# Optimization experiments

Hardware: AMD Instinct MI355X
Metric: run time of the kernel (lower is better)

Reference implementation:

```python
import jax, jax.numpy as jnp
import numpy as np

N_NODES = 100000


def _graph_conv(x, W, b, src, dst, inv_sqrt_out, inv_sqrt_in):
    # DGL GraphConv, norm='both':  D_in^{-1/2} A D_out^{-1/2} X W + b
    h = x * inv_sqrt_out[:, None]
    if W.shape[0] > W.shape[1]:
        # in_feats > out_feats: transform first (cheaper aggregation)
        h = h @ W
        m = jax.ops.segment_sum(h[src], dst, num_segments=N_NODES)
    else:
        m = jax.ops.segment_sum(h[src], dst, num_segments=N_NODES)
        m = m @ W
    return m * inv_sqrt_in[:, None] + b


def _degree_norms(src, dst):
    ones = jnp.ones(src.shape[0], dtype=jnp.float32)
    out_deg = jax.ops.segment_sum(ones, src, num_segments=N_NODES)
    in_deg = jax.ops.segment_sum(ones, dst, num_segments=N_NODES)
    # DGL clamps degree to min 1 (allow_zero_in_degree)
    return jnp.clip(out_deg, 1.0) ** -0.5, jnp.clip(in_deg, 1.0) ** -0.5


def setup_inputs() -> dict:
    key = jax.random.key(0)
    ks = jax.random.split(key, 8)
    E = 800000
    in_feats, h1, h2, nc = 128, 256, 128, 40
    return {
        "features": jax.random.normal(ks[0], (N_NODES, in_feats), dtype=jnp.float32),
        "src": jax.random.randint(ks[1], (E,), 0, N_NODES),
        "dst": jax.random.randint(ks[2], (E,), 0, N_NODES),
        "W1": jax.random.normal(ks[3], (in_feats, h1), dtype=jnp.float32) * (2.0 / (in_feats + h1)) ** 0.5,
        "b1": jnp.zeros((h1,), dtype=jnp.float32),
        "W2": jax.random.normal(ks[4], (h1, h2), dtype=jnp.float32) * (2.0 / (h1 + h2)) ** 0.5,
        "b2": jnp.zeros((h2,), dtype=jnp.float32),
        "W3": jax.random.normal(ks[5], (h2, nc), dtype=jnp.float32) * (2.0 / (h2 + nc)) ** 0.5,
        "b3": jnp.zeros((nc,), dtype=jnp.float32),
    }


def reference(features, src, dst, W1, b1, W2, b2, W3, b3):
    inv_out, inv_in = _degree_norms(src, dst)
    h = _graph_conv(features, W1, b1, src, dst, inv_out, inv_in)
    h = jax.nn.relu(h)
    h = _graph_conv(h, W2, b2, src, dst, inv_out, inv_in)
    h = jax.nn.relu(h)
    return _graph_conv(h, W3, b3, src, dst, inv_out, inv_in)
```

## Files before the change

kernel.cpp:

```cpp
#include <hip/hip_runtime.h>

#define N_NODES 100000
#define SCAN_NB 128
#define SCAN_TPB 256
#define GCOUNT 8
#define BINS 12500
#define NSLICE 32

typedef _Float16 half_t;
typedef __attribute__((ext_vector_type(8))) _Float16 v8h;
typedef __attribute__((ext_vector_type(4))) _Float16 v4h;
typedef __attribute__((ext_vector_type(4))) float v4f;


__global__ __launch_bounds__(512) void hist_all(
    const int* __restrict__ src, const int* __restrict__ dst,
    int* __restrict__ loc, unsigned short* __restrict__ partialI,
    unsigned short* __restrict__ partialO, int E,
    const float* __restrict__ W1, const float* __restrict__ W2,
    const float* __restrict__ W3, half_t* __restrict__ Wt1,
    half_t* __restrict__ Wt2, half_t* __restrict__ Wt3) {
    __shared__ int hist[BINS];
    const int bid = blockIdx.x;
    const int tid = threadIdx.x;
    if (bid < 2 * GCOUNT * NSLICE) {
        const bool isDst = bid < GCOUNT * NSLICE;
        const int b2 = isDst ? bid : bid - GCOUNT * NSLICE;
        const int g = b2 >> 5, s = b2 & (NSLICE - 1);
        const int gbase = g * BINS;
        for (int b = tid; b < BINS; b += 512) hist[b] = 0;
        __syncthreads();
        const int chunk = (E + NSLICE - 1) / NSLICE;
        const int e0 = s * chunk;
        const int e1 = min(e0 + chunk, E);
        if (isDst) {
            for (int e = e0 + tid; e < e1; e += 512) {
                int d = dst[e];
                unsigned lb = (unsigned)(d - gbase);
                if (lb < (unsigned)BINS) loc[e] = atomicAdd(&hist[lb], 1);
            }
        } else {
            for (int e = e0 + tid; e < e1; e += 512) {
                int d = src[e];
                unsigned lb = (unsigned)(d - gbase);
                if (lb < (unsigned)BINS) atomicAdd(&hist[lb], 1);
            }
        }
        __syncthreads();
        unsigned short* p = (isDst ? partialI : partialO) + (size_t)b2 * BINS;
        for (int b = tid; b < BINS; b += 512) p[b] = (unsigned short)hist[b];
    } else {
        int u = (bid - 2 * GCOUNT * NSLICE) * 512 + tid;
        if (u < 32768) {
            int n = u >> 7, k = u & 127;
            Wt1[u] = (half_t)W1[(size_t)k * 256 + n];
        } else if (u < 65536) {
            int w = u - 32768;
            int n = w >> 8, k = w & 255;
            Wt2[w] = (half_t)W2[(size_t)k * 128 + n];
        } else if (u < 70656) {
            int w = u - 65536;
            int n = w >> 7, k = w & 127;
            Wt3[w] = (half_t)W3[(size_t)k * 40 + n];
        }
    }
}


__global__ __launch_bounds__(SCAN_TPB) void scan_reduce(
    const unsigned short* __restrict__ partialI, int* __restrict__ blockSum, int n) {
    __shared__ int s[SCAN_TPB];
    int chunk = (n + SCAN_NB - 1) / SCAN_NB;
    int beg = blockIdx.x * chunk;
    int end = min(beg + chunk, n);
    int sum = 0;
    for (int i = beg + threadIdx.x; i < end; i += SCAN_TPB) {
        int g = i / BINS, lb = i - g * BINS;
        const unsigned short* p = partialI + (size_t)g * NSLICE * BINS + lb;
#pragma unroll
        for (int sl = 0; sl < NSLICE; ++sl) sum += p[(size_t)sl * BINS];
    }
    s[threadIdx.x] = sum;
    __syncthreads();
    for (int off = SCAN_TPB / 2; off > 0; off >>= 1) {
        if (threadIdx.x < off) s[threadIdx.x] += s[threadIdx.x + off];
        __syncthreads();
    }
    if (threadIdx.x == 0) blockSum[blockIdx.x] = s[0];
}

__global__ __launch_bounds__(SCAN_NB) void scan_offsets(int* __restrict__ blockSum,
                                                        int* __restrict__ rowptr_total) {
    __shared__ int s[SCAN_NB];
    int tid = threadIdx.x;
    int v = blockSum[tid];
    s[tid] = v;
    __syncthreads();
    for (int off = 1; off < SCAN_NB; off <<= 1) {
        int t = (tid >= off) ? s[tid - off] : 0;
        __syncthreads();
        s[tid] += t;
        __syncthreads();
    }
    blockSum[tid] = s[tid] - v;
    if (tid == SCAN_NB - 1) rowptr_total[0] = s[tid];
}

__global__ __launch_bounds__(SCAN_TPB) void scan_final(
    unsigned short* __restrict__ partialI, const unsigned short* __restrict__ partialO,
    const int* __restrict__ blockSum, int* __restrict__ rowptr,
    float* __restrict__ invIn, float* __restrict__ invOut, int n) {
    __shared__ int s[SCAN_TPB];
    int chunk = (n + SCAN_NB - 1) / SCAN_NB;
    int beg = blockIdx.x * chunk;
    int end = min(beg + chunk, n);
    int carry = blockSum[blockIdx.x];
    for (int base = beg; base < end; base += SCAN_TPB) {
        int i = base + threadIdx.x;
        int v = 0, o = 0;
        if (i < end) {
            int g = i / BINS, lb = i - g * BINS;
            unsigned short* p = partialI + (size_t)g * NSLICE * BINS + lb;
            int run = 0;
#pragma unroll
            for (int sl = 0; sl < NSLICE; ++sl) {
                int c = p[(size_t)sl * BINS];
                p[(size_t)sl * BINS] = (unsigned short)run;
                run += c;
            }
            v = run;
            const unsigned short* q = partialO + (size_t)g * NSLICE * BINS + lb;
#pragma unroll
            for (int sl = 0; sl < NSLICE; ++sl) o += q[(size_t)sl * BINS];
        }
        s[threadIdx.x] = v;
        __syncthreads();
        for (int off = 1; off < SCAN_TPB; off <<= 1) {
            int t = (threadIdx.x >= off) ? s[threadIdx.x - off] : 0;
            __syncthreads();
            s[threadIdx.x] += t;
            __syncthreads();
        }
        int excl = s[threadIdx.x] - v;
        if (i < end) {
            rowptr[i] = carry + excl;
            invOut[i] = rsqrtf((float)max(o, 1));
            invIn[i] = rsqrtf((float)max(v, 1));
        }
        int roundSum = s[SCAN_TPB - 1];
        __syncthreads();
        carry += roundSum;
    }
}


__global__ void prep2(const int* __restrict__ src, const int* __restrict__ dst,
                      const int* __restrict__ loc,
                      const unsigned short* __restrict__ partialI,
                      const int* __restrict__ rowptr,
                      int* __restrict__ eidx, int E,
                      const float* __restrict__ x, const float* __restrict__ invOut,
                      half_t* __restrict__ xh) {
    int t = blockIdx.x * blockDim.x + threadIdx.x;
    if (t < E) {
        int d = dst[t];
        int chunk = (E + NSLICE - 1) / NSLICE;
        int s = t / chunk;
        int g = d / BINS, lb = d - g * BINS;
        int pre = partialI[(size_t)(g * NSLICE + s) * BINS + lb];
        eidx[rowptr[d] + pre + loc[t]] = src[t];
    } else {
        int u = t - E;
        if (u < N_NODES * 32) {
            int n = u >> 5;
            float4 v = ((const float4*)x)[u];
            float s = invOut[n];
            v4h h;
            h[0] = (half_t)(v.x * s);
            h[1] = (half_t)(v.y * s);
            h[2] = (half_t)(v.z * s);
            h[3] = (half_t)(v.w * s);
            *(v4h*)(xh + (size_t)u * 4) = h;
        }
    }
}


template <int F>
__device__ __forceinline__ void gather_row(const half_t* __restrict__ x,
                                           const int* __restrict__ eidx,
                                           int beg, int end, int c, float* acc) {
    const half_t* __restrict__ xc = x + (size_t)c * 8;
    int n = end - beg;
    if (n <= 0) return;
    int nbat = (n + 3) >> 2;
    int i0 = eidx[beg];
    int i1 = eidx[beg + min(1, n - 1)];
    int i2 = eidx[beg + min(2, n - 1)];
    int i3 = eidx[beg + min(3, n - 1)];
    for (int b = 0; b < nbat; ++b) {
        int j = b * 4;
        v8h v0 = *(const v8h*)(xc + (size_t)i0 * F);
        v8h v1 = *(const v8h*)(xc + (size_t)i1 * F);
        v8h v2 = *(const v8h*)(xc + (size_t)i2 * F);
        v8h v3 = *(const v8h*)(xc + (size_t)i3 * F);
        if (b + 1 < nbat) {
            int jn = j + 4;
            i0 = eidx[beg + jn];
            i1 = eidx[beg + min(jn + 1, n - 1)];
            i2 = eidx[beg + min(jn + 2, n - 1)];
            i3 = eidx[beg + min(jn + 3, n - 1)];
        }
        v8h z = (v8h)(half_t)0;
        v1 = (j + 1 < n) ? v1 : z;
        v2 = (j + 2 < n) ? v2 : z;
        v3 = (j + 3 < n) ? v3 : z;
#pragma unroll
        for (int q = 0; q < 8; ++q)
            acc[q] += ((float)v0[q] + (float)v1[q]) + ((float)v2[q] + (float)v3[q]);
    }
}


__global__ __launch_bounds__(256, 8) void gather1(
    const half_t* __restrict__ xh, const int* __restrict__ rowptr,
    const int* __restrict__ eidx, half_t* __restrict__ A1) {
    int t = blockIdx.x * 256 + threadIdx.x;
    int n = t >> 4, c = t & 15;
    if (n >= N_NODES) return;
    float acc[8] = {};
    gather_row<128>(xh, eidx, rowptr[n], rowptr[n + 1], c, acc);
    v8h o;
#pragma unroll
    for (int q = 0; q < 8; ++q) o[q] = (half_t)acc[q];
    *(v8h*)(A1 + (size_t)n * 128 + c * 8) = o;
}

__global__ __launch_bounds__(256, 8) void gather2(
    const half_t* __restrict__ t2, const int* __restrict__ rowptr,
    const int* __restrict__ eidx, const float* __restrict__ invIn,
    const float* __restrict__ invOut, const float* __restrict__ b2,
    half_t* __restrict__ A2) {
    int t = blockIdx.x * 256 + threadIdx.x;
    int n = t >> 4, c = t & 15;
    if (n >= N_NODES) return;
    float acc[8] = {};
    gather_row<128>(t2, eidx, rowptr[n], rowptr[n + 1], c, acc);
    float ii = invIn[n], io = invOut[n];
    float4 blo = ((const float4*)b2)[c * 2];
    float4 bhi = ((const float4*)b2)[c * 2 + 1];
    float bb[8] = {blo.x, blo.y, blo.z, blo.w, bhi.x, bhi.y, bhi.z, bhi.w};
    v8h o;
#pragma unroll
    for (int q = 0; q < 8; ++q)
        o[q] = (half_t)fmaxf((acc[q] * ii + bb[q]) * io, 0.f);
    *(v8h*)(A2 + (size_t)n * 128 + c * 8) = o;
}


__global__ __launch_bounds__(512) void mlp12(
    const half_t* __restrict__ A1, const half_t* __restrict__ Wt1,
    const half_t* __restrict__ Wt2,
    const float* __restrict__ invIn, const float* __restrict__ invOut,
    const float* __restrict__ b1, half_t* __restrict__ t2) {
    constexpr int K1 = 128, K2 = 256, N2 = 128;
    constexpr int LDA = K1 + 8;
    constexpr int LDH = K2 + 8;
    __shared__ half_t As[64][LDA];
    __shared__ half_t h1S[64][LDH];
    __shared__ float iiS[64], ioS[64];
    const int tid = threadIdx.x;
    const int wave = tid >> 6, lane = tid & 63;
    const int quad = lane >> 4, l16 = lane & 15;
    const int m0 = blockIdx.x * 64;
    const int n0 = wave * 32;

    v8h b[2][4];
    float bv[2];
#pragma unroll
    for (int j = 0; j < 2; ++j) {
        int gn = n0 + j * 16 + l16;
        bv[j] = b1[gn];
#pragma unroll
        for (int kc = 0; kc < 4; ++kc)
            b[j][kc] = *(const v8h*)(Wt1 + (size_t)gn * K1 + kc * 32 + quad * 8);
    }
    if (tid < 64) {
        int gm = m0 + tid;
        bool ok = gm < N_NODES;
        iiS[tid] = ok ? invIn[gm] : 0.f;
        ioS[tid] = ok ? invOut[gm] : 0.f;
    }

#pragma unroll
    for (int p = 0; p < 2; ++p) {
        int task = tid + p * 512;
        int r = task >> 4, c = task & 15;
        int gm = m0 + r;
        v8h v = (gm < N_NODES) ? *(const v8h*)(A1 + (size_t)gm * K1 + c * 8)
                               : (v8h)(half_t)0;
        *(v8h*)&As[r][c * 8] = v;
    }
    __syncthreads();

    for (int mt = 0; mt < 4; ++mt) {
        v8h a[4];
#pragma unroll
        for (int kc = 0; kc < 4; ++kc)
            a[kc] = *(const v8h*)&As[mt * 16 + l16][kc * 32 + quad * 8];
        v4f acc[2] = {};
#pragma unroll
        for (int kc = 0; kc < 4; ++kc)
#pragma unroll
            for (int j = 0; j < 2; ++j)
                acc[j] = __builtin_amdgcn_mfma_f32_16x16x32_f16(a[kc], b[j][kc], acc[j], 0, 0, 0);
#pragma unroll
        for (int j = 0; j < 2; ++j) {
            int cn = n0 + j * 16 + l16;
#pragma unroll
            for (int r = 0; r < 4; ++r) {
                int lr = mt * 16 + quad * 4 + r;
                float z = (acc[j][r] * iiS[lr] + bv[j]) * ioS[lr];
                h1S[lr][cn] = (half_t)fmaxf(z, 0.f);
            }
        }
    }

    v8h b2[8];
    const int n02 = wave * 16;
    {
        int gn = n02 + l16;
#pragma unroll
        for (int kc = 0; kc < 8; ++kc)
            b2[kc] = *(const v8h*)(Wt2 + (size_t)gn * K2 + kc * 32 + quad * 8);
    }
    __syncthreads();

    for (int mt = 0; mt < 4; ++mt) {
        v8h a2[8];
#pragma unroll
        for (int kc = 0; kc < 8; ++kc)
            a2[kc] = *(const v8h*)&h1S[mt * 16 + l16][kc * 32 + quad * 8];
        v4f acc2 = {};
#pragma unroll
        for (int kc = 0; kc < 8; ++kc)
            acc2 = __builtin_amdgcn_mfma_f32_16x16x32_f16(a2[kc], b2[kc], acc2, 0, 0, 0);
        int gn = n02 + l16;
#pragma unroll
        for (int r = 0; r < 4; ++r) {
            int gm = m0 + mt * 16 + quad * 4 + r;
            if (gm < N_NODES) t2[(size_t)gm * N2 + gn] = (half_t)acc2[r];
        }
    }
}


__global__ __launch_bounds__(256) void mlp3(
    const half_t* __restrict__ A2, const half_t* __restrict__ Wt3,
    half_t* __restrict__ t3) {
    constexpr int K = 128, N = 40, LDA = K + 8;
    __shared__ half_t As[64][LDA];
    const int tid = threadIdx.x;
    const int wave = tid >> 6, lane = tid & 63;
    const int quad = lane >> 4, l16 = lane & 15;
    const int m0 = blockIdx.x * 64;

    v8h b[3][4];
#pragma unroll
    for (int j = 0; j < 3; ++j) {
        int gn = j * 16 + l16;
#pragma unroll
        for (int kc = 0; kc < 4; ++kc)
            b[j][kc] = (gn < N) ? *(const v8h*)(Wt3 + (size_t)gn * K + kc * 32 + quad * 8)
                                : (v8h)(half_t)0;
    }

#pragma unroll
    for (int p = 0; p < 4; ++p) {
        int task = tid + p * 256;
        int r = task >> 4, c = task & 15;
        int gm = m0 + r;
        v8h v = (gm < N_NODES) ? *(const v8h*)(A2 + (size_t)gm * K + c * 8)
                               : (v8h)(half_t)0;
        *(v8h*)&As[r][c * 8] = v;
    }
    __syncthreads();

    {
        int mt = wave;
        v8h a[4];
#pragma unroll
        for (int kc = 0; kc < 4; ++kc)
            a[kc] = *(const v8h*)&As[mt * 16 + l16][kc * 32 + quad * 8];
        v4f acc[3] = {};
#pragma unroll
        for (int kc = 0; kc < 4; ++kc)
#pragma unroll
            for (int j = 0; j < 3; ++j)
                acc[j] = __builtin_amdgcn_mfma_f32_16x16x32_f16(a[kc], b[j][kc], acc[j], 0, 0, 0);
#pragma unroll
        for (int j = 0; j < 3; ++j) {
            int gn = j * 16 + l16;
            if (gn >= N) continue;
#pragma unroll
            for (int r = 0; r < 4; ++r) {
                int gm = m0 + mt * 16 + quad * 4 + r;
                if (gm < N_NODES) t3[(size_t)gm * N + gn] = (half_t)acc[j][r];
            }
        }
    }
}


__global__ __launch_bounds__(256, 8) void gather_final(
    const half_t* __restrict__ x,
    const int* __restrict__ rowptr, const int* __restrict__ eidx,
    float* __restrict__ out, const float* __restrict__ invIn,
    const float* __restrict__ bias) {
    constexpr int F = 40, V = 5;
    int t = blockIdx.x * blockDim.x + threadIdx.x;
    int n = t / V;
    int v = t - n * V;
    if (n >= N_NODES) return;
    float acc[8] = {};
    gather_row<F>(x, eidx, rowptr[n], rowptr[n + 1], v, acc);
    float ii = invIn[n];
    float* o = out + (size_t)n * F + v * 8;
#pragma unroll
    for (int q = 0; q < 8; ++q) o[q] = acc[q] * ii + bias[v * 8 + q];
}


extern "C" void kernel_launch(void* const* d_in, const int* in_sizes, int n_in,
                              void* d_out, int out_size, void* d_ws, size_t ws_size,
                              hipStream_t stream) {
    const float* x  = (const float*)d_in[0];
    const int* src  = (const int*)d_in[1];
    const int* dst  = (const int*)d_in[2];
    const float* W1 = (const float*)d_in[3];
    const float* b1 = (const float*)d_in[4];
    const float* W2 = (const float*)d_in[5];
    const float* b2 = (const float*)d_in[6];
    const float* W3 = (const float*)d_in[7];
    const float* b3 = (const float*)d_in[8];
    float* out = (float*)d_out;
    const int E = in_sizes[1];

    char* ws = (char*)d_ws;
    float* inv_out = (float*)ws;
    float* inv_in  = (float*)(ws + 400000);
    int* rowptr    = (int*)(ws + 800000);
    int* eidx      = (int*)(ws + 1600256);
    int* blockSum  = (int*)(ws + 4800256);
    half_t* Wt1    = (half_t*)(ws + 4800768);
    half_t* Wt2    = (half_t*)(ws + 4866304);
    half_t* Wt3    = (half_t*)(ws + 4931840);
    half_t* bufA   = (half_t*)(ws + 5000192);
    half_t* bufB   = (half_t*)(ws + 30600192);
    int* loc = (int*)bufB;
    unsigned short* partialI = (unsigned short*)((char*)bufB + 3200000);
    unsigned short* partialO = partialI + (size_t)GCOUNT * NSLICE * BINS;

    const int NBH = 2 * GCOUNT * NSLICE + (70656 + 511) / 512;
    hist_all<<<NBH, 512, 0, stream>>>(src, dst, loc, partialI, partialO, E,
                                      W1, W2, W3, Wt1, Wt2, Wt3);
    scan_reduce<<<SCAN_NB, SCAN_TPB, 0, stream>>>(partialI, blockSum, N_NODES);
    scan_offsets<<<1, SCAN_NB, 0, stream>>>(blockSum, rowptr + N_NODES);
    scan_final<<<SCAN_NB, SCAN_TPB, 0, stream>>>(partialI, partialO, blockSum, rowptr,
                                                 inv_in, inv_out, N_NODES);
    prep2<<<(E + N_NODES * 32 + 255) / 256, 256, 0, stream>>>(src, dst, loc, partialI,
                                                              rowptr, eidx, E,
                                                              x, inv_out, bufA);

    const int NBG = (N_NODES * 16 + 255) / 256;
    const int NB  = (N_NODES + 63) / 64;

    gather1<<<NBG, 256, 0, stream>>>(bufA, rowptr, eidx, bufB);
    mlp12<<<NB, 512, 0, stream>>>(bufB, Wt1, Wt2, inv_in, inv_out, b1, bufA);
    gather2<<<NBG, 256, 0, stream>>>(bufA, rowptr, eidx, inv_in, inv_out, b2, bufB);
    mlp3<<<NB, 256, 0, stream>>>(bufB, Wt3, bufA);
    gather_final<<<(N_NODES * 5 + 255) / 256, 256, 0, stream>>>(
        bufA, rowptr, eidx, out, inv_in, b3);
}
```

Baseline: 294.4 us.

## Fuse layer-2 gather with layer-3 weight transform into one kernel

Merges gather2 and mlp3 into a single kernel. Each 512-thread block gathers 32 rows into shared memory, then six waves apply the 128x40 MFMA transform. This removes the write and read of the 100000x128 half-precision intermediate A2 and one kernel launch. The cost is a block-wide barrier after an irregular gather, so waves stall on the slowest row, and two of the eight waves sit idle in the MFMA phase.

```diff
diff --git a/kernel.cpp b/kernel.cpp
--- a/kernel.cpp
+++ b/kernel.cpp
@@ -236,25 +236,68 @@
     *(v8h*)(A1 + (size_t)n * 128 + c * 8) = o;
 }
 
-__global__ __launch_bounds__(256, 8) void gather2(
+
+__global__ __launch_bounds__(512) void gather2t3(
     const half_t* __restrict__ t2, const int* __restrict__ rowptr,
     const int* __restrict__ eidx, const float* __restrict__ invIn,
     const float* __restrict__ invOut, const float* __restrict__ b2,
-    half_t* __restrict__ A2) {
-    int t = blockIdx.x * 256 + threadIdx.x;
-    int n = t >> 4, c = t & 15;
-    if (n >= N_NODES) return;
-    float acc[8] = {};
-    gather_row<128>(t2, eidx, rowptr[n], rowptr[n + 1], c, acc);
-    float ii = invIn[n], io = invOut[n];
-    float4 blo = ((const float4*)b2)[c * 2];
-    float4 bhi = ((const float4*)b2)[c * 2 + 1];
-    float bb[8] = {blo.x, blo.y, blo.z, blo.w, bhi.x, bhi.y, bhi.z, bhi.w};
-    v8h o;
-#pragma unroll
-    for (int q = 0; q < 8; ++q)
-        o[q] = (half_t)fmaxf((acc[q] * ii + bb[q]) * io, 0.f);
-    *(v8h*)(A2 + (size_t)n * 128 + c * 8) = o;
+    const half_t* __restrict__ Wt3, half_t* __restrict__ t3) {
+    constexpr int K = 128, N = 40, LDA = K + 8;
+    __shared__ half_t As[32][LDA];
+    const int tid = threadIdx.x;
+    const int wave = tid >> 6, lane = tid & 63;
+    const int quad = lane >> 4, l16 = lane & 15;
+    const int m0 = blockIdx.x * 32;
+    const int mt = wave & 1, jn = wave >> 1;
+
+    v8h b[4];
+    if (jn < 3) {
+        int gn = jn * 16 + l16;
+#pragma unroll
+        for (int kc = 0; kc < 4; ++kc)
+            b[kc] = (gn < N) ? *(const v8h*)(Wt3 + (size_t)gn * K + kc * 32 + quad * 8)
+                             : (v8h)(half_t)0;
+    }
+
+    {
+        int r = tid >> 4, c = tid & 15;
+        int n = m0 + r;
+        float acc[8] = {};
+        float ii = 0.f, io = 0.f;
+        if (n < N_NODES) {
+            ii = invIn[n];
+            io = invOut[n];
+            gather_row<128>(t2, eidx, rowptr[n], rowptr[n + 1], c, acc);
+        }
+        float4 blo = ((const float4*)b2)[c * 2];
+        float4 bhi = ((const float4*)b2)[c * 2 + 1];
+        float bb[8] = {blo.x, blo.y, blo.z, blo.w, bhi.x, bhi.y, bhi.z, bhi.w};
+        v8h o;
+#pragma unroll
+        for (int q = 0; q < 8; ++q)
+            o[q] = (half_t)fmaxf((acc[q] * ii + bb[q]) * io, 0.f);
+        *(v8h*)&As[r][c * 8] = o;
+    }
+    __syncthreads();
+
+    if (jn < 3) {
+        v8h a[4];
+#pragma unroll
+        for (int kc = 0; kc < 4; ++kc)
+            a[kc] = *(const v8h*)&As[mt * 16 + l16][kc * 32 + quad * 8];
+        v4f acc = {};
+#pragma unroll
+        for (int kc = 0; kc < 4; ++kc)
+            acc = __builtin_amdgcn_mfma_f32_16x16x32_f16(a[kc], b[kc], acc, 0, 0, 0);
+        int gn = jn * 16 + l16;
+        if (gn < N) {
+#pragma unroll
+            for (int r = 0; r < 4; ++r) {
+                int gm = m0 + mt * 16 + quad * 4 + r;
+                if (gm < N_NODES) t3[(size_t)gm * N + gn] = (half_t)acc[r];
+            }
+        }
+    }
 }
 
 
@@ -355,63 +398,6 @@
 }
 
 
-__global__ __launch_bounds__(256) void mlp3(
-    const half_t* __restrict__ A2, const half_t* __restrict__ Wt3,
-    half_t* __restrict__ t3) {
-    constexpr int K = 128, N = 40, LDA = K + 8;
-    __shared__ half_t As[64][LDA];
-    const int tid = threadIdx.x;
-    const int wave = tid >> 6, lane = tid & 63;
-    const int quad = lane >> 4, l16 = lane & 15;
-    const int m0 = blockIdx.x * 64;
-
-    v8h b[3][4];
-#pragma unroll
-    for (int j = 0; j < 3; ++j) {
-        int gn = j * 16 + l16;
-#pragma unroll
-        for (int kc = 0; kc < 4; ++kc)
-            b[j][kc] = (gn < N) ? *(const v8h*)(Wt3 + (size_t)gn * K + kc * 32 + quad * 8)
-                                : (v8h)(half_t)0;
-    }
-
-#pragma unroll
-    for (int p = 0; p < 4; ++p) {
-        int task = tid + p * 256;
-        int r = task >> 4, c = task & 15;
-        int gm = m0 + r;
-        v8h v = (gm < N_NODES) ? *(const v8h*)(A2 + (size_t)gm * K + c * 8)
-                               : (v8h)(half_t)0;
-        *(v8h*)&As[r][c * 8] = v;
-    }
-    __syncthreads();
-
-    {
-        int mt = wave;
-        v8h a[4];
-#pragma unroll
-        for (int kc = 0; kc < 4; ++kc)
-            a[kc] = *(const v8h*)&As[mt * 16 + l16][kc * 32 + quad * 8];
-        v4f acc[3] = {};
-#pragma unroll
-        for (int kc = 0; kc < 4; ++kc)
-#pragma unroll
-            for (int j = 0; j < 3; ++j)
-                acc[j] = __builtin_amdgcn_mfma_f32_16x16x32_f16(a[kc], b[j][kc], acc[j], 0, 0, 0);
-#pragma unroll
-        for (int j = 0; j < 3; ++j) {
-            int gn = j * 16 + l16;
-            if (gn >= N) continue;
-#pragma unroll
-            for (int r = 0; r < 4; ++r) {
-                int gm = m0 + mt * 16 + quad * 4 + r;
-                if (gm < N_NODES) t3[(size_t)gm * N + gn] = (half_t)acc[j][r];
-            }
-        }
-    }
-}
-
-
 __global__ __launch_bounds__(256, 8) void gather_final(
     const half_t* __restrict__ x,
     const int* __restrict__ rowptr, const int* __restrict__ eidx,
@@ -474,11 +460,11 @@
 
     const int NBG = (N_NODES * 16 + 255) / 256;
     const int NB  = (N_NODES + 63) / 64;
+    const int NBF = (N_NODES + 31) / 32;
 
     gather1<<<NBG, 256, 0, stream>>>(bufA, rowptr, eidx, bufB);
     mlp12<<<NB, 512, 0, stream>>>(bufB, Wt1, Wt2, inv_in, inv_out, b1, bufA);
-    gather2<<<NBG, 256, 0, stream>>>(bufA, rowptr, eidx, inv_in, inv_out, b2, bufB);
-    mlp3<<<NB, 256, 0, stream>>>(bufB, Wt3, bufA);
+    gather2t3<<<NBF, 512, 0, stream>>>(bufA, rowptr, eidx, inv_in, inv_out, b2, Wt3, bufB);
     gather_final<<<(N_NODES * 5 + 255) / 256, 256, 0, stream>>>(
-        bufA, rowptr, eidx, out, inv_in, b3);
-}
+        bufB, rowptr, eidx, out, inv_in, b3);
+}
```

Result: faster. 283.4 us, median of 2 (-3.7%).
